# Kernel tuning notes

Measured on AMD Instinct MI355X. Metric: run time of the kernel, lower is better.

Reference implementation:

```python
import jax, jax.numpy as jnp
from jax import lax
import numpy as np

D_MODEL = 1024; N_HEADS = 16; D_K = 64; D_FF = 4096
D_STATE = 16; D_CONV = 4; D_INNER = 2048; EPS = 1e-5
BATCH = 2; SEQ = 2048


def _ln(x, g, b):
    m = x.mean(-1, keepdims=True)
    v = ((x - m) ** 2).mean(-1, keepdims=True)
    return (x - m) * lax.rsqrt(v + EPS) * g + b


def setup_inputs() -> dict:
    key = jax.random.key(0)
    ks = jax.random.split(key, 12)
    rn = lambda k, sh, s=0.02: jax.random.normal(k, sh, jnp.float32) * s
    return {
        'x': jax.random.normal(ks[0], (BATCH, SEQ, D_MODEL), jnp.float32),
        'ln1_g': jnp.ones(D_MODEL), 'ln1_b': jnp.zeros(D_MODEL),
        'Wq': rn(ks[1], (D_MODEL, D_MODEL)), 'bq': jnp.zeros(D_MODEL),
        'Wk': rn(ks[2], (D_MODEL, D_MODEL)), 'bk': jnp.zeros(D_MODEL),
        'Wv': rn(ks[3], (D_MODEL, D_MODEL)), 'bv': jnp.zeros(D_MODEL),
        'Wo': rn(ks[4], (D_MODEL, D_MODEL)), 'bo': jnp.zeros(D_MODEL),
        'ln2_g': jnp.ones(D_MODEL), 'ln2_b': jnp.zeros(D_MODEL),
        'in_w': rn(ks[5], (D_MODEL, 2 * D_INNER)), 'in_b': jnp.zeros(2 * D_INNER),
        'conv_w': rn(ks[6], (D_INNER, 1, D_CONV), 0.2), 'conv_b': jnp.zeros(D_INNER),
        'xp_w': rn(ks[7], (D_INNER, 2 * D_STATE)), 'xp_b': jnp.zeros(2 * D_STATE),
        'dt': rn(ks[8], (D_INNER,), 0.1), 'A': rn(ks[9], (D_STATE, D_STATE), 0.1),
        'Dp': jnp.ones(D_INNER),
        'out_w': rn(ks[10], (D_INNER, D_MODEL)), 'out_b': jnp.zeros(D_MODEL),
        'ln3_g': jnp.ones(D_MODEL), 'ln3_b': jnp.zeros(D_MODEL),
        'fc1_w': rn(ks[11], (D_MODEL, D_FF)), 'fc1_b': jnp.zeros(D_FF),
        'fc2_w': rn(jax.random.fold_in(key, 99), (D_FF, D_MODEL)), 'fc2_b': jnp.zeros(D_MODEL),
    }


def reference(x, ln1_g, ln1_b, Wq, bq, Wk, bk, Wv, bv, Wo, bo, ln2_g, ln2_b,
              in_w, in_b, conv_w, conv_b, xp_w, xp_b, dt, A, Dp, out_w, out_b,
              ln3_g, ln3_b, fc1_w, fc1_b, fc2_w, fc2_b):
    Bsz, S, _ = x.shape
    # --- attention (block sliding-window mask == full causal mask) ---
    h = _ln(x, ln1_g, ln1_b)
    q = (h @ Wq + bq).reshape(Bsz, S, N_HEADS, D_K).transpose(0, 2, 1, 3)
    k = (h @ Wk + bk).reshape(Bsz, S, N_HEADS, D_K).transpose(0, 2, 1, 3)
    v = (h @ Wv + bv).reshape(Bsz, S, N_HEADS, D_K).transpose(0, 2, 1, 3)
    scores = jnp.einsum('bhqd,bhkd->bhqk', q, k) / float(D_K ** 0.5)
    causal = jnp.tril(jnp.ones((S, S), bool))
    scores = jnp.where(causal, scores, -jnp.inf)
    probs = jax.nn.softmax(scores, axis=-1)
    attn = jnp.einsum('bhqk,bhkd->bhqd', probs, v).transpose(0, 2, 1, 3).reshape(Bsz, S, D_MODEL)
    x = x + attn @ Wo + bo
    # --- Mamba-style layer ---
    h = _ln(x, ln2_g, ln2_b)
    xr = h @ in_w + in_b                      # (B,S,2*Di)
    xm, res = xr[..., :D_INNER], xr[..., D_INNER:]
    # causal depthwise conv: torch Conv1d(pad=d_conv-1)[..., :S] == left-pad conv
    xc = lax.conv_general_dilated(xm.transpose(0, 2, 1), conv_w, (1,), [(D_CONV - 1, 0)],
                                  dimension_numbers=('NCH', 'OIH', 'NCH'),
                                  feature_group_count=D_INNER)
    xm = jax.nn.silu((xc + conv_b[None, :, None]).transpose(0, 2, 1))
    xdbl = xm @ xp_w + xp_b                   # (B,S,2*d_state)
    Bm, Cm = xdbl[..., :D_STATE], xdbl[..., D_STATE:]
    # dt = exp(param)[:d_state], indexed by i % d_state per step (as in source)
    dts = jnp.exp(dt)[:D_STATE][jnp.arange(S) % D_STATE]  # (S,)
    # NOTE: the source scan never uses u = x[:,i,:] (and hence D); hs depends
    # only on dt, A, B, C — replicated faithfully here.

    def step(hst, inp):
        d_t, b_t, c_t = inp
        A_t = jnp.exp(d_t * A)                # (d_state,d_state)
        hst = jnp.tanh(hst @ A_t.T) + b_t * hst + c_t
        return hst, hst

    h0 = jnp.zeros((Bsz, D_STATE), x.dtype)
    _, hs = lax.scan(step, h0, (dts, Bm.transpose(1, 0, 2), Cm.transpose(1, 0, 2)))
    hs = hs.transpose(1, 0, 2)                # (B,S,d_state)
    y = jnp.repeat(hs, D_INNER // D_STATE, axis=-1) + res
    x = x + y @ out_w + out_b
    # --- FFN (tanh-approx GELU) ---
    h = _ln(x, ln3_g, ln3_b)
    x = x + jax.nn.gelu(h @ fc1_w + fc1_b, approximate=True) @ fc2_w + fc2_b
    return x
```

## Files before the change

kernel.cpp:

```cpp
#include <hip/hip_runtime.h>
#include <hip/hip_bf16.h>


#define SEQ     2048
#define BATCH   2
#define MROWS   4096
#define DMODEL  1024
#define DINNER  2048
#define DFF     4096
#define QKVLD   3072

typedef __attribute__((ext_vector_type(8))) short bf16x8;
typedef __attribute__((ext_vector_type(4))) float f32x4;

__device__ __forceinline__ unsigned short f2b(float x){
    __hip_bfloat16 h = __float2bfloat16(x);
    return *reinterpret_cast<unsigned short*>(&h);
}
__device__ __forceinline__ float b2f(unsigned short u){
    __hip_bfloat16 h;
    *reinterpret_cast<unsigned short*>(&h) = u;
    return __bfloat162float(h);
}
__device__ __forceinline__ float b2f_lo(unsigned u){
    return __builtin_bit_cast(float, u << 16);
}
__device__ __forceinline__ float b2f_hi(unsigned u){
    return __builtin_bit_cast(float, u & 0xFFFF0000u);
}
__device__ __forceinline__ float gelu_f(float v){
    float u = 0.7978845608f*(v + 0.044715f*v*v*v);
    float e = __expf(2.f*u);
    float th = 1.f - 2.f*__builtin_amdgcn_rcpf(e + 1.f);
    return 0.5f*v*(1.f + th);
}
__device__ __forceinline__ void gload16(const unsigned short* g, unsigned short* l){
    __builtin_amdgcn_global_load_lds(
        (const __attribute__((address_space(1))) void*)g,
        (__attribute__((address_space(3))) void*)l, 16, 0, 0);
}
__device__ __forceinline__ void gload16f(const float* g, float* l){
    __builtin_amdgcn_global_load_lds(
        (const __attribute__((address_space(1))) void*)g,
        (__attribute__((address_space(3))) void*)l, 16, 0, 0);
}
template<int CTRL>
__device__ __forceinline__ float dppf(float x){
    int r = __builtin_amdgcn_mov_dpp(__builtin_bit_cast(int, x), CTRL, 0xf, 0xf, false);
    return __builtin_bit_cast(float, r);
}
template<int CTRL>
__device__ __forceinline__ int dppi(int x){
    return __builtin_amdgcn_mov_dpp(x, CTRL, 0xf, 0xf, false);
}

__global__ __launch_bounds__(256) void transpose_cast(
    const float* __restrict__ W, unsigned short* __restrict__ Wt, int K, int N)
{
    __shared__ float t[64*65];
    int n0 = blockIdx.x*64, k0 = blockIdx.y*64;
    int c = threadIdx.x & 63, r0 = threadIdx.x >> 6;
    #pragma unroll
    for (int rr = 0; rr < 64; rr += 4)
        t[(rr+r0)*65 + c] = W[(size_t)(k0+rr+r0)*N + n0 + c];
    __syncthreads();
    #pragma unroll
    for (int rr = 0; rr < 64; rr += 4)
        Wt[(size_t)(n0+rr+r0)*K + k0 + c] = f2b(t[c*65 + rr + r0]);
}

__global__ __launch_bounds__(256) void concat_bias(
    const float* __restrict__ b0, const float* __restrict__ b1,
    const float* __restrict__ b2, float* __restrict__ o)
{
    int t = blockIdx.x*256 + threadIdx.x;
    float v = (t < 1024) ? b0[t] : (t < 2048 ? b1[t-1024] : b2[t-2048]);
    o[t] = v;
}

__global__ __launch_bounds__(256) void layernorm_bf16(
    const float* __restrict__ x, const float* __restrict__ g,
    const float* __restrict__ b, unsigned short* __restrict__ out)
{
    int row = blockIdx.x;
    const float4* xr = (const float4*)(x + (size_t)row*DMODEL);
    int tid = threadIdx.x;
    float4 xv = xr[tid];
    float s  = xv.x + xv.y + xv.z + xv.w;
    float ss = xv.x*xv.x + xv.y*xv.y + xv.z*xv.z + xv.w*xv.w;
    #pragma unroll
    for (int d = 32; d > 0; d >>= 1){ s += __shfl_xor(s,d); ss += __shfl_xor(ss,d); }
    __shared__ float sm[8];
    int wv = tid>>6, ln = tid&63;
    if (ln == 0){ sm[wv] = s; sm[4+wv] = ss; }
    __syncthreads();
    s  = sm[0]+sm[1]+sm[2]+sm[3];
    ss = sm[4]+sm[5]+sm[6]+sm[7];
    float mean = s*(1.f/DMODEL);
    float var  = ss*(1.f/DMODEL) - mean*mean;
    float rstd = rsqrtf(var + 1e-5f);
    float4 gv = ((const float4*)g)[tid];
    float4 bv = ((const float4*)b)[tid];
    ushort4 o;
    o.x = f2b((xv.x-mean)*rstd*gv.x + bv.x);
    o.y = f2b((xv.y-mean)*rstd*gv.y + bv.y);
    o.z = f2b((xv.z-mean)*rstd*gv.z + bv.z);
    o.w = f2b((xv.w-mean)*rstd*gv.w + bv.w);
    ((ushort4*)(out + (size_t)row*DMODEL))[tid] = o;
}

template<int BN, int OUT_BF16, int HAS_RES, int ACT>
__global__ __launch_bounds__(256,2) void gemm_bt(
    const unsigned short* __restrict__ A, const unsigned short* __restrict__ Bt,
    const float* __restrict__ bias, const float* __restrict__ res,
    void* __restrict__ outp, int Ndim, int Kdim)
{
    constexpr int NT = BN/32;
    constexpr int BROWS = BN/32;
    __shared__ unsigned short As[128*64];
    __shared__ unsigned short Bs[BN*64];
    int tid = threadIdx.x;
    int lane = tid & 63, wv = tid >> 6;
    int l15 = lane & 15, quad = lane >> 4;
    int m0 = blockIdx.y*128, n0 = blockIdx.x*BN;
    int mo = (wv>>1)*64, no = (wv&1)*(BN/2);
    int rsub = (lane >> 3);
    int cc8  = (lane & 7)*8;
    f32x4 zz = {0.f,0.f,0.f,0.f};
    f32x4 acc[4][NT];
    #pragma unroll
    for (int i=0;i<4;++i)
      #pragma unroll
      for (int j=0;j<NT;++j) acc[i][j] = zz;

    for (int k0 = 0; k0 < Kdim; k0 += 64){
        const unsigned short* Ab = A  + (size_t)(m0 + wv*32 + rsub)*Kdim + k0 + cc8;
        const unsigned short* Bb = Bt + (size_t)(n0 + wv*(BN/4) + rsub)*Kdim + k0 + cc8;
        #pragma unroll
        for (int i=0;i<4;++i)
            gload16(Ab + (size_t)(i*8)*Kdim, &As[(wv*32 + i*8)*64]);
        #pragma unroll
        for (int i=0;i<BROWS;++i)
            gload16(Bb + (size_t)(i*8)*Kdim, &Bs[(wv*(BN/4) + i*8)*64]);
        __syncthreads();
        #pragma unroll
        for (int kc=0;kc<2;++kc){
            bf16x8 af[4], bfr[NT];
            #pragma unroll
            for (int t=0;t<4;++t)
                af[t]  = *(const bf16x8*)(&As[(mo + t*16 + l15)*64 + kc*32 + quad*8]);
            #pragma unroll
            for (int t=0;t<NT;++t)
                bfr[t] = *(const bf16x8*)(&Bs[(no + t*16 + l15)*64 + kc*32 + quad*8]);
            #pragma unroll
            for (int mt=0;mt<4;++mt)
              #pragma unroll
              for (int nt=0;nt<NT;++nt)
                acc[mt][nt] = __builtin_amdgcn_mfma_f32_16x16x32_bf16(af[mt], bfr[nt], acc[mt][nt], 0,0,0);
        }
        __syncthreads();
    }
    #pragma unroll
    for (int mt=0;mt<4;++mt){
      #pragma unroll
      for (int nt=0;nt<NT;++nt){
        int gn = n0 + no + nt*16 + l15;
        float bval = bias[gn];
        #pragma unroll
        for (int r=0;r<4;++r){
            int gm = m0 + mo + mt*16 + quad*4 + r;
            size_t off = (size_t)gm*Ndim + gn;
            float v = acc[mt][nt][r] + bval;
            if constexpr (HAS_RES) v += res[off];
            if constexpr (ACT == 1) v = gelu_f(v);
            if constexpr (OUT_BF16) ((unsigned short*)outp)[off] = f2b(v);
            else                    ((float*)outp)[off] = v;
        }
      }
    }
}

__global__ __launch_bounds__(256,2) void attn_flash(
    const unsigned short* __restrict__ qkv, unsigned short* __restrict__ attn)
{
    __shared__ unsigned short Qs[64*72];
    __shared__ unsigned short Ks[64*72];
    __shared__ unsigned short Vt[64*72];
    __shared__ unsigned short Ps[64*72];
    int bh = blockIdx.y;
    int qt = (int)gridDim.x - 1 - (int)blockIdx.x;
    int q0 = qt*64;
    int tid = threadIdx.x, wv = tid>>6, lane = tid&63;
    int l15 = lane&15, quad = lane>>4;
    const size_t basei = (size_t)(bh>>4)*SEQ*QKVLD + (size_t)(bh&15)*64;
    const unsigned short* q = qkv + basei;
    const unsigned short* k = qkv + basei + DMODEL;
    const unsigned short* v = qkv + basei + 2*DMODEL;
    const size_t baseo = (size_t)(bh>>4)*SEQ*DMODEL + (size_t)(bh&15)*64;

    #pragma unroll
    for (int i=0;i<2;++i){
        int cch = tid + i*256; int r = cch>>3, cc = cch&7;
        *(uint4*)(&Qs[r*72 + cc*8]) = *(const uint4*)(q + (size_t)(q0+r)*QKVLD + cc*8);
    }
    __syncthreads();
    bf16x8 aq0 = *(const bf16x8*)(&Qs[(wv*16 + l15)*72 + quad*8]);
    bf16x8 aq1 = *(const bf16x8*)(&Qs[(wv*16 + l15)*72 + 32 + quad*8]);

    float m_i[4], l_i[4];
    f32x4 zz = {0.f,0.f,0.f,0.f};
    f32x4 o[4];
    #pragma unroll
    for (int r=0;r<4;++r){ m_i[r] = -__builtin_inff(); l_i[r] = 0.f; }
    #pragma unroll
    for (int d=0;d<4;++d) o[d] = zz;

    for (int kt = 0; kt <= qt; ++kt){
        int t0 = kt*64;
        #pragma unroll
        for (int i=0;i<2;++i){
            int cch = tid + i*256; int r = cch>>3, cc = cch&7;
            *(uint4*)(&Ks[r*72 + cc*8]) = *(const uint4*)(k + (size_t)(t0+r)*QKVLD + cc*8);
            uint4 vv = *(const uint4*)(v + (size_t)(t0+r)*QKVLD + cc*8);
            const unsigned short* pv = (const unsigned short*)&vv;
            #pragma unroll
            for (int j=0;j<8;++j) Vt[(cc*8+j)*72 + r] = pv[j];
        }
        __syncthreads();

        f32x4 sc[4];
        #pragma unroll
        for (int st=0;st<4;++st){
            bf16x8 b0 = *(const bf16x8*)(&Ks[(st*16+l15)*72 + quad*8]);
            bf16x8 b1 = *(const bf16x8*)(&Ks[(st*16+l15)*72 + 32 + quad*8]);
            sc[st] = __builtin_amdgcn_mfma_f32_16x16x32_bf16(aq0, b0, zz, 0,0,0);
            sc[st] = __builtin_amdgcn_mfma_f32_16x16x32_bf16(aq1, b1, sc[st], 0,0,0);
        }
        bool diag = (kt == qt);
        float sval[4][4];
        float mrow[4];
        #pragma unroll
        for (int r=0;r<4;++r) mrow[r] = -__builtin_inff();
        #pragma unroll
        for (int st=0;st<4;++st)
          #pragma unroll
          for (int r=0;r<4;++r){
            float svv = sc[st][r]*0.125f;
            if (diag && (st*16 + l15 > wv*16 + quad*4 + r)) svv = -__builtin_inff();
            sval[st][r] = svv;
            mrow[r] = fmaxf(mrow[r], svv);
          }
        #pragma unroll
        for (int d=1; d<16; d<<=1)
          #pragma unroll
          for (int r=0;r<4;++r) mrow[r] = fmaxf(mrow[r], __shfl_xor(mrow[r], d));
        float alpha[4], rsum[4];
        #pragma unroll
        for (int r=0;r<4;++r){
            float mn = fmaxf(m_i[r], mrow[r]);
            alpha[r] = __expf(m_i[r] - mn);
            m_i[r] = mn;
        }
        #pragma unroll
        for (int st=0;st<4;++st)
          #pragma unroll
          for (int r=0;r<4;++r) sval[st][r] = __expf(sval[st][r] - m_i[r]);
        #pragma unroll
        for (int r=0;r<4;++r) rsum[r] = sval[0][r]+sval[1][r]+sval[2][r]+sval[3][r];
        #pragma unroll
        for (int d=1; d<16; d<<=1)
          #pragma unroll
          for (int r=0;r<4;++r) rsum[r] += __shfl_xor(rsum[r], d);
        #pragma unroll
        for (int r=0;r<4;++r) l_i[r] = l_i[r]*alpha[r] + rsum[r];
        #pragma unroll
        for (int st=0;st<4;++st)
          #pragma unroll
          for (int r=0;r<4;++r)
            Ps[(wv*16 + quad*4 + r)*72 + st*16 + l15] = f2b(sval[st][r]);
        #pragma unroll
        for (int d=0;d<4;++d)
          #pragma unroll
          for (int r=0;r<4;++r) o[d][r] = o[d][r]*alpha[r];
        __syncthreads();
        bf16x8 ap0 = *(const bf16x8*)(&Ps[(wv*16 + l15)*72 + quad*8]);
        bf16x8 ap1 = *(const bf16x8*)(&Ps[(wv*16 + l15)*72 + 32 + quad*8]);
        #pragma unroll
        for (int dtile=0;dtile<4;++dtile){
            bf16x8 b0 = *(const bf16x8*)(&Vt[(dtile*16+l15)*72 + quad*8]);
            bf16x8 b1 = *(const bf16x8*)(&Vt[(dtile*16+l15)*72 + 32 + quad*8]);
            o[dtile] = __builtin_amdgcn_mfma_f32_16x16x32_bf16(ap0, b0, o[dtile], 0,0,0);
            o[dtile] = __builtin_amdgcn_mfma_f32_16x16x32_bf16(ap1, b1, o[dtile], 0,0,0);
        }
        __syncthreads();
    }
    #pragma unroll
    for (int r=0;r<4;++r){
        float inv = 1.f/l_i[r];
        int gm = q0 + wv*16 + quad*4 + r;
        #pragma unroll
        for (int dtile=0;dtile<4;++dtile)
            attn[baseo + (size_t)gm*DMODEL + dtile*16 + l15] = f2b(o[dtile][r]*inv);
    }
}

__global__ __launch_bounds__(256) void conv_silu(
    const unsigned short* __restrict__ xr, const float* __restrict__ cw,
    const float* __restrict__ cb, unsigned short* __restrict__ xm2)
{
    int idx = blockIdx.x*256 + threadIdx.x;
    int r  = idx >> 10;
    int c2 = (idx & 1023)*2;
    int s  = r & (SEQ-1);
    float4 w0 = *(const float4*)(cw + c2*4);
    float4 w1 = *(const float4*)(cw + (c2+1)*4);
    float w0a[4] = {w0.x,w0.y,w0.z,w0.w};
    float w1a[4] = {w1.x,w1.y,w1.z,w1.w};
    float a0 = cb[c2], a1 = cb[c2+1];
    const unsigned short* xrow = xr + (size_t)r*DFF + c2;
    #pragma unroll
    for (int j=0;j<4;++j){
        int sp = s - 3 + j;
        if (sp >= 0){
            int off = (j-3)*DFF;
            unsigned int u = *(const unsigned int*)(xrow + off);
            a0 += w0a[j]*b2f(u & 0xffff);
            a1 += w1a[j]*b2f(u >> 16);
        }
    }
    float s0 = a0 * __builtin_amdgcn_rcpf(1.f + __expf(-a0));
    float s1 = a1 * __builtin_amdgcn_rcpf(1.f + __expf(-a1));
    unsigned int op = (unsigned int)f2b(s0) | ((unsigned int)f2b(s1) << 16);
    *(unsigned int*)(xm2 + (size_t)r*DINNER + c2) = op;
}

__global__ __launch_bounds__(256) void xp_gemm(
    const unsigned short* __restrict__ xm2, const float* __restrict__ w,
    const float* __restrict__ bias, float* __restrict__ xdbl)
{
    int tid = threadIdx.x;
    int lr = tid >> 5, n = tid & 31;
    int row = blockIdx.x*8 + lr;
    const unsigned short* ar = xm2 + (size_t)row*DINNER;
    float acc = bias[n];
    #pragma unroll 4
    for (int k2 = 0; k2 < DINNER; k2 += 2){
        unsigned int u = *(const unsigned int*)(ar + k2);
        acc += b2f(u & 0xffff)*w[k2*32 + n] + b2f(u >> 16)*w[(k2+1)*32 + n];
    }
    int nc = (n < 16) ? 2*n : 2*(n-16)+1;
    xdbl[(size_t)row*32 + nc] = acc;
}

__device__ __forceinline__ float scan_step_pk(float h, const unsigned (&Wp)[8],
                                              float bv, float cv)
{
    float r1  = dppf<0x121>(h);
    float r2  = dppf<0x122>(h);
    float r3  = dppf<0x123>(h);
    float r4  = dppf<0x124>(h);
    float r5  = dppf<0x125>(h);
    float r6  = dppf<0x126>(h);
    float r7  = dppf<0x127>(h);
    float r8  = dppf<0x128>(h);
    float r9  = dppf<0x129>(h);
    float r10 = dppf<0x12a>(h);
    float r11 = dppf<0x12b>(h);
    float r12 = dppf<0x12c>(h);
    float r13 = dppf<0x12d>(h);
    float r14 = dppf<0x12e>(h);
    float r15 = dppf<0x12f>(h);
    float a0 = b2f_lo(Wp[0])*h;
    a0 = fmaf(b2f_hi(Wp[0]), r1, a0);
    a0 = fmaf(b2f_lo(Wp[1]), r2, a0);
    a0 = fmaf(b2f_hi(Wp[1]), r3, a0);
    float a1 = b2f_lo(Wp[2])*r4;
    a1 = fmaf(b2f_hi(Wp[2]), r5, a1);
    a1 = fmaf(b2f_lo(Wp[3]), r6, a1);
    a1 = fmaf(b2f_hi(Wp[3]), r7, a1);
    float a2 = b2f_lo(Wp[4])*r8;
    a2 = fmaf(b2f_hi(Wp[4]), r9, a2);
    a2 = fmaf(b2f_lo(Wp[5]), r10, a2);
    a2 = fmaf(b2f_hi(Wp[5]), r11, a2);
    float a3 = b2f_lo(Wp[6])*r12;
    a3 = fmaf(b2f_hi(Wp[6]), r13, a3);
    a3 = fmaf(b2f_lo(Wp[7]), r14, a3);
    a3 = fmaf(b2f_hi(Wp[7]), r15, a3);
    float x = (a0+a1)+(a2+a3);
    float e2 = __expf(x);
    float th = 1.f - 2.f*__builtin_amdgcn_rcpf(e2 + 1.f);
    return th + fmaf(bv, h, cv);
}

__global__ __launch_bounds__(128,1) void scan_k(
    const float* __restrict__ xdbl, const float* __restrict__ dt,
    const float* __restrict__ A, float* __restrict__ hsT)
{
    __shared__ float bc[2][2][64*32];
    int tid = threadIdx.x;
    int wv = tid >> 6, lane = tid & 63;
    int i = lane & 15;
    int b = wv;

    int c[16];
    c[0]  = i;
    c[1]  = dppi<0x121>(i);
    c[2]  = dppi<0x122>(i);
    c[3]  = dppi<0x123>(i);
    c[4]  = dppi<0x124>(i);
    c[5]  = dppi<0x125>(i);
    c[6]  = dppi<0x126>(i);
    c[7]  = dppi<0x127>(i);
    c[8]  = dppi<0x128>(i);
    c[9]  = dppi<0x129>(i);
    c[10] = dppi<0x12a>(i);
    c[11] = dppi<0x12b>(i);
    c[12] = dppi<0x12c>(i);
    c[13] = dppi<0x12d>(i);
    c[14] = dppi<0x12e>(i);
    c[15] = dppi<0x12f>(i);

    unsigned Wpk[16][8];
    #pragma unroll
    for (int p=0;p<16;++p){
        float dtp = __expf(dt[p]);
        #pragma unroll
        for (int jj=0;jj<8;++jj){
            float w0 = 2.f*__expf(dtp * A[i*16 + c[2*jj]]);
            float w1 = 2.f*__expf(dtp * A[i*16 + c[2*jj+1]]);
            Wpk[p][jj] = (unsigned)f2b(w0) | ((unsigned)f2b(w1) << 16);
        }
    }

    {
        const float* src = xdbl + (size_t)(b*SEQ)*32 + lane*4;
        #pragma unroll
        for (int k=0;k<8;++k)
            gload16f(src + k*256, &bc[wv][0][k*256]);
    }
    __builtin_amdgcn_s_waitcnt(0x0F70);

    float hn = 0.f;
    float h0s=0.f, h1s=0.f, h2s=0.f;
    for (int chunk = 0; chunk < 32; ++chunk){
        if (chunk < 31){
            const float* nsrc = xdbl + (size_t)(b*SEQ + (chunk+1)*64)*32 + lane*4;
            float* nb = &bc[wv][(chunk+1)&1][0];
            #pragma unroll
            for (int k=0;k<8;++k)
                gload16f(nsrc + k*256, nb + k*256);
        }
        const float* cur = &bc[wv][chunk&1][0];
        float* hp = hsT + (size_t)(b*16 + i)*SEQ + chunk*64;
        float2 bc0 = *(const float2*)(cur + 2*i);
        float2 bc1 = *(const float2*)(cur + 32 + 2*i);
        #pragma unroll
        for (int st=0; st<64; ++st){
            float bv = bc0.x, cv = bc0.y;
            bc0 = bc1;
            if (st < 62)
                bc1 = *(const float2*)(cur + (st+2)*32 + 2*i);
            hn = scan_step_pk(hn, Wpk[st & 15], bv, cv);
            if ((st&3)==0)      h0s = hn;
            else if ((st&3)==1) h1s = hn;
            else if ((st&3)==2) h2s = hn;
            else if (lane < 16){
                float4 o4 = {h0s, h1s, h2s, hn};
                *(float4*)(hp + (st-3)) = o4;
            }
        }
        __builtin_amdgcn_s_waitcnt(0x0F70);
    }
}

__global__ __launch_bounds__(256) void y_assemble(
    const float* __restrict__ hsT, const unsigned short* __restrict__ xr,
    unsigned short* __restrict__ y)
{
    int idx = blockIdx.x*256 + threadIdx.x;
    int r = idx >> 10;
    int c2 = (idx & 1023)*2;
    int bb = r >> 11, s = r & (SEQ-1);
    unsigned int u = *(const unsigned int*)(xr + (size_t)r*DFF + DINNER + c2);
    float h0 = hsT[(size_t)(bb*16 + (c2 >> 7))*SEQ + s];
    float y0 = h0 + b2f(u & 0xffff);
    float y1 = h0 + b2f(u >> 16);
    *(unsigned int*)(y + (size_t)r*DINNER + c2) =
        (unsigned int)f2b(y0) | ((unsigned int)f2b(y1) << 16);
}

extern "C" void kernel_launch(void* const* d_in, const int* in_sizes, int n_in,
                              void* d_out, int out_size, void* d_ws, size_t ws_size,
                              hipStream_t stream)
{
    (void)in_sizes; (void)n_in; (void)out_size; (void)ws_size;
    const float* x     = (const float*)d_in[0];
    const float* ln1_g = (const float*)d_in[1];
    const float* ln1_b = (const float*)d_in[2];
    const float* Wq    = (const float*)d_in[3];
    const float* bq    = (const float*)d_in[4];
    const float* Wk    = (const float*)d_in[5];
    const float* bk    = (const float*)d_in[6];
    const float* Wv    = (const float*)d_in[7];
    const float* bv    = (const float*)d_in[8];
    const float* Wo    = (const float*)d_in[9];
    const float* bo    = (const float*)d_in[10];
    const float* ln2_g = (const float*)d_in[11];
    const float* ln2_b = (const float*)d_in[12];
    const float* in_w  = (const float*)d_in[13];
    const float* in_b  = (const float*)d_in[14];
    const float* conv_w= (const float*)d_in[15];
    const float* conv_b= (const float*)d_in[16];
    const float* xp_w  = (const float*)d_in[17];
    const float* xp_b  = (const float*)d_in[18];
    const float* dt    = (const float*)d_in[19];
    const float* A     = (const float*)d_in[20];
    const float* out_w = (const float*)d_in[22];
    const float* out_b = (const float*)d_in[23];
    const float* ln3_g = (const float*)d_in[24];
    const float* ln3_b = (const float*)d_in[25];
    const float* fc1_w = (const float*)d_in[26];
    const float* fc1_b = (const float*)d_in[27];
    const float* fc2_w = (const float*)d_in[28];
    const float* fc2_b = (const float*)d_in[29];

    char* ws = (char*)d_ws;
    const size_t MB = 1ull << 20;
    unsigned short* qkvT = (unsigned short*)(ws + 0*MB);
    unsigned short* WoT  = (unsigned short*)(ws + 6*MB);
    unsigned short* inT  = (unsigned short*)(ws + 8*MB);
    unsigned short* outT = (unsigned short*)(ws + 16*MB);
    unsigned short* f1T  = (unsigned short*)(ws + 20*MB);
    unsigned short* f2T  = (unsigned short*)(ws + 28*MB);
    unsigned short* hbf  = (unsigned short*)(ws + 36*MB);
    float*          x2   = (float*)(ws + 44*MB);
    float*          x3   = (float*)(ws + 60*MB);
    unsigned short* qkv  = (unsigned short*)(ws + 76*MB);
    unsigned short* attnb= (unsigned short*)(ws + 100*MB);
    unsigned short* xr   = (unsigned short*)(ws + 76*MB);
    unsigned short* ffn  = (unsigned short*)(ws + 76*MB);
    unsigned short* xm2  = (unsigned short*)(ws + 108*MB);
    unsigned short* yb   = (unsigned short*)(ws + 108*MB);
    float*          xdbl = (float*)(ws + 124*MB);
    float*          hsb  = (float*)(ws + 124*MB + 512*1024);
    float*          bqkv = (float*)(ws + 125*MB);

    dim3 blk(256);
    transpose_cast<<<dim3(16,16), blk, 0, stream>>>(Wq, qkvT,              1024, 1024);
    transpose_cast<<<dim3(16,16), blk, 0, stream>>>(Wk, qkvT + 1024*1024,  1024, 1024);
    transpose_cast<<<dim3(16,16), blk, 0, stream>>>(Wv, qkvT + 2*1024*1024,1024, 1024);
    transpose_cast<<<dim3(16,16), blk, 0, stream>>>(Wo, WoT, 1024, 1024);
    transpose_cast<<<dim3(64,16), blk, 0, stream>>>(in_w, inT, 1024, 4096);
    transpose_cast<<<dim3(16,32), blk, 0, stream>>>(out_w, outT, 2048, 1024);
    transpose_cast<<<dim3(64,16), blk, 0, stream>>>(fc1_w, f1T, 1024, 4096);
    transpose_cast<<<dim3(16,64), blk, 0, stream>>>(fc2_w, f2T, 4096, 1024);
    concat_bias<<<12, blk, 0, stream>>>(bq, bk, bv, bqkv);

    layernorm_bf16<<<MROWS, blk, 0, stream>>>(x, ln1_g, ln1_b, hbf);
    gemm_bt<128,1,0,0><<<dim3(24,32), blk, 0, stream>>>(hbf, qkvT, bqkv, nullptr, qkv, QKVLD, 1024);
    attn_flash<<<dim3(32,32), blk, 0, stream>>>(qkv, attnb);
    gemm_bt<64,0,1,0><<<dim3(16,32), blk, 0, stream>>>(attnb, WoT, bo, x, x2, 1024, 1024);
    layernorm_bf16<<<MROWS, blk, 0, stream>>>(x2, ln2_g, ln2_b, hbf);
    gemm_bt<128,1,0,0><<<dim3(32,32), blk, 0, stream>>>(hbf, inT, in_b, nullptr, xr, 4096, 1024);
    conv_silu<<<16384, blk, 0, stream>>>(xr, conv_w, conv_b, xm2);
    xp_gemm<<<512, blk, 0, stream>>>(xm2, xp_w, xp_b, xdbl);
    scan_k<<<1, dim3(128), 0, stream>>>(xdbl, dt, A, hsb);
    y_assemble<<<16384, blk, 0, stream>>>(hsb, xr, yb);
    gemm_bt<64,0,1,0><<<dim3(16,32), blk, 0, stream>>>(yb, outT, out_b, x2, x3, 1024, 2048);
    layernorm_bf16<<<MROWS, blk, 0, stream>>>(x3, ln3_g, ln3_b, hbf);
    gemm_bt<128,1,0,1><<<dim3(32,32), blk, 0, stream>>>(hbf, f1T, fc1_b, nullptr, ffn, 4096, 1024);
    gemm_bt<64,0,1,0><<<dim3(16,32), blk, 0, stream>>>(ffn, f2T, fc2_b, x3, (float*)d_out, 1024, 4096);
}
```

Baseline: 997.1 us.

## Use packed fp16 dot2 and DPP pairs in serial scan step, register-prefetch inputs

Rewrites the per-step recurrence of the sequential scan to pack the state into fp16 pairs. It shuffles them with 7 DPP moves instead of 15 and accumulates with v_dot2 instructions. The weights are pre-scaled so that exp2 can replace exp, and the tanh is folded into one rcp plus one fma. The LDS double-buffer for B/C is replaced by direct global loads into register banks that are prefetched 16 steps ahead. The aim is to shorten the latency-bound critical path of the serial scan, at the cost of fp16 rounding of the state and weights.

```diff
diff --git a/kernel.cpp b/kernel.cpp
--- a/kernel.cpp
+++ b/kernel.cpp
@@ -12,6 +12,7 @@
 
 typedef __attribute__((ext_vector_type(8))) short bf16x8;
 typedef __attribute__((ext_vector_type(4))) float f32x4;
+typedef __attribute__((ext_vector_type(2))) __fp16 f16x2;
 
 __device__ __forceinline__ unsigned short f2b(float x){
     __hip_bfloat16 h = __float2bfloat16(x);
@@ -21,12 +22,6 @@
     __hip_bfloat16 h;
     *reinterpret_cast<unsigned short*>(&h) = u;
     return __bfloat162float(h);
-}
-__device__ __forceinline__ float b2f_lo(unsigned u){
-    return __builtin_bit_cast(float, u << 16);
-}
-__device__ __forceinline__ float b2f_hi(unsigned u){
-    return __builtin_bit_cast(float, u & 0xFFFF0000u);
 }
 __device__ __forceinline__ float gelu_f(float v){
     float u = 0.7978845608f*(v + 0.044715f*v*v*v);
@@ -39,11 +34,6 @@
         (const __attribute__((address_space(1))) void*)g,
         (__attribute__((address_space(3))) void*)l, 16, 0, 0);
 }
-__device__ __forceinline__ void gload16f(const float* g, float* l){
-    __builtin_amdgcn_global_load_lds(
-        (const __attribute__((address_space(1))) void*)g,
-        (__attribute__((address_space(3))) void*)l, 16, 0, 0);
-}
 template<int CTRL>
 __device__ __forceinline__ float dppf(float x){
     int r = __builtin_amdgcn_mov_dpp(__builtin_bit_cast(int, x), CTRL, 0xf, 0xf, false);
@@ -52,6 +42,27 @@
 template<int CTRL>
 __device__ __forceinline__ int dppi(int x){
     return __builtin_amdgcn_mov_dpp(x, CTRL, 0xf, 0xf, false);
+}
+template<int CTRL>
+__device__ __forceinline__ f16x2 dpp_h2(f16x2 x){
+    int r = __builtin_amdgcn_mov_dpp(__builtin_bit_cast(int, x), CTRL, 0xf, 0xf, false);
+    return __builtin_bit_cast(f16x2, r);
+}
+
+#if __has_builtin(__builtin_amdgcn_exp2f)
+#define W_SCALE 2.8853900817779268f
+__device__ __forceinline__ float exp_2s(float x){ return __builtin_amdgcn_exp2f(x); }
+#else
+#define W_SCALE 2.0f
+__device__ __forceinline__ float exp_2s(float x){ return __expf(x); }
+#endif
+
+__device__ __forceinline__ float hdot2(f16x2 a, f16x2 b, float c){
+#if __has_builtin(__builtin_amdgcn_fdot2)
+    return __builtin_amdgcn_fdot2(a, b, c, false);
+#else
+    return c + (float)a[0]*(float)b[0] + (float)a[1]*(float)b[1];
+#endif
 }
 
 __global__ __launch_bounds__(256) void transpose_cast(
@@ -352,124 +363,99 @@
     xdbl[(size_t)row*32 + nc] = acc;
 }
 
-__device__ __forceinline__ float scan_step_pk(float h, const unsigned (&Wp)[8],
-                                              float bv, float cv)
-{
-    float r1  = dppf<0x121>(h);
-    float r2  = dppf<0x122>(h);
-    float r3  = dppf<0x123>(h);
-    float r4  = dppf<0x124>(h);
-    float r5  = dppf<0x125>(h);
-    float r6  = dppf<0x126>(h);
-    float r7  = dppf<0x127>(h);
-    float r8  = dppf<0x128>(h);
-    float r9  = dppf<0x129>(h);
-    float r10 = dppf<0x12a>(h);
-    float r11 = dppf<0x12b>(h);
-    float r12 = dppf<0x12c>(h);
-    float r13 = dppf<0x12d>(h);
-    float r14 = dppf<0x12e>(h);
-    float r15 = dppf<0x12f>(h);
-    float a0 = b2f_lo(Wp[0])*h;
-    a0 = fmaf(b2f_hi(Wp[0]), r1, a0);
-    a0 = fmaf(b2f_lo(Wp[1]), r2, a0);
-    a0 = fmaf(b2f_hi(Wp[1]), r3, a0);
-    float a1 = b2f_lo(Wp[2])*r4;
-    a1 = fmaf(b2f_hi(Wp[2]), r5, a1);
-    a1 = fmaf(b2f_lo(Wp[3]), r6, a1);
-    a1 = fmaf(b2f_hi(Wp[3]), r7, a1);
-    float a2 = b2f_lo(Wp[4])*r8;
-    a2 = fmaf(b2f_hi(Wp[4]), r9, a2);
-    a2 = fmaf(b2f_lo(Wp[5]), r10, a2);
-    a2 = fmaf(b2f_hi(Wp[5]), r11, a2);
-    float a3 = b2f_lo(Wp[6])*r12;
-    a3 = fmaf(b2f_hi(Wp[6]), r13, a3);
-    a3 = fmaf(b2f_lo(Wp[7]), r14, a3);
-    a3 = fmaf(b2f_hi(Wp[7]), r15, a3);
-    float x = (a0+a1)+(a2+a3);
-    float e2 = __expf(x);
-    float th = 1.f - 2.f*__builtin_amdgcn_rcpf(e2 + 1.f);
-    return th + fmaf(bv, h, cv);
+__device__ __forceinline__ float scan_step_dot(float h, const f16x2 (&Wp)[8],
+                                               float bv, float cv)
+{
+    float rr = dppf<0x121>(h);
+    f16x2 p0 = __builtin_amdgcn_cvt_pkrtz(h, rr);
+    f16x2 p1 = dpp_h2<0x122>(p0);
+    f16x2 p2 = dpp_h2<0x124>(p0);
+    f16x2 p3 = dpp_h2<0x126>(p0);
+    f16x2 p4 = dpp_h2<0x128>(p0);
+    f16x2 p5 = dpp_h2<0x12a>(p0);
+    f16x2 p6 = dpp_h2<0x12c>(p0);
+    f16x2 p7 = dpp_h2<0x12e>(p0);
+    float a0 = hdot2(Wp[0], p0, 0.f);
+    a0 = hdot2(Wp[1], p1, a0);
+    a0 = hdot2(Wp[2], p2, a0);
+    a0 = hdot2(Wp[3], p3, a0);
+    float a1 = hdot2(Wp[4], p4, 0.f);
+    a1 = hdot2(Wp[5], p5, a1);
+    a1 = hdot2(Wp[6], p6, a1);
+    a1 = hdot2(Wp[7], p7, a1);
+    float u  = fmaf(bv, h, cv + 1.f);
+    float e2 = exp_2s(a0 + a1);
+    float r  = __builtin_amdgcn_rcpf(e2 + 1.f);
+    return fmaf(-2.f, r, u);
+}
+
+__device__ __forceinline__ void load_bank(float2 (&bk)[16], const float* src){
+    #pragma unroll
+    for (int j=0;j<16;++j) bk[j] = *(const float2*)(src + (size_t)j*32);
+}
+
+__device__ __forceinline__ void compute16(const float2 (&bk)[16],
+                                          const f16x2 (&Wf)[16][8],
+                                          float& hn, float* hp, int lane)
+{
+    float h0s=0.f, h1s=0.f, h2s=0.f;
+    #pragma unroll
+    for (int j=0;j<16;++j){
+        hn = scan_step_dot(hn, Wf[j], bk[j].x, bk[j].y);
+        if ((j&3)==0)      h0s = hn;
+        else if ((j&3)==1) h1s = hn;
+        else if ((j&3)==2) h2s = hn;
+        else if (lane < 16){
+            float4 o4 = {h0s, h1s, h2s, hn};
+            *(float4*)(hp + j - 3) = o4;
+        }
+    }
 }
 
 __global__ __launch_bounds__(128,1) void scan_k(
     const float* __restrict__ xdbl, const float* __restrict__ dt,
     const float* __restrict__ A, float* __restrict__ hsT)
 {
-    __shared__ float bc[2][2][64*32];
     int tid = threadIdx.x;
-    int wv = tid >> 6, lane = tid & 63;
+    int lane = tid & 63;
+    int b = tid >> 6;
     int i = lane & 15;
-    int b = wv;
-
-    int c[16];
-    c[0]  = i;
-    c[1]  = dppi<0x121>(i);
-    c[2]  = dppi<0x122>(i);
-    c[3]  = dppi<0x123>(i);
-    c[4]  = dppi<0x124>(i);
-    c[5]  = dppi<0x125>(i);
-    c[6]  = dppi<0x126>(i);
-    c[7]  = dppi<0x127>(i);
-    c[8]  = dppi<0x128>(i);
-    c[9]  = dppi<0x129>(i);
-    c[10] = dppi<0x12a>(i);
-    c[11] = dppi<0x12b>(i);
-    c[12] = dppi<0x12c>(i);
-    c[13] = dppi<0x12d>(i);
-    c[14] = dppi<0x12e>(i);
-    c[15] = dppi<0x12f>(i);
-
-    unsigned Wpk[16][8];
+
+    int c1 = dppi<0x121>(i);
+    int sj[8], tj[8];
+    sj[0] = i;               tj[0] = c1;
+    sj[1] = dppi<0x122>(i);  tj[1] = dppi<0x122>(c1);
+    sj[2] = dppi<0x124>(i);  tj[2] = dppi<0x124>(c1);
+    sj[3] = dppi<0x126>(i);  tj[3] = dppi<0x126>(c1);
+    sj[4] = dppi<0x128>(i);  tj[4] = dppi<0x128>(c1);
+    sj[5] = dppi<0x12a>(i);  tj[5] = dppi<0x12a>(c1);
+    sj[6] = dppi<0x12c>(i);  tj[6] = dppi<0x12c>(c1);
+    sj[7] = dppi<0x12e>(i);  tj[7] = dppi<0x12e>(c1);
+
+    f16x2 Wf[16][8];
     #pragma unroll
     for (int p=0;p<16;++p){
         float dtp = __expf(dt[p]);
         #pragma unroll
         for (int jj=0;jj<8;++jj){
-            float w0 = 2.f*__expf(dtp * A[i*16 + c[2*jj]]);
-            float w1 = 2.f*__expf(dtp * A[i*16 + c[2*jj+1]]);
-            Wpk[p][jj] = (unsigned)f2b(w0) | ((unsigned)f2b(w1) << 16);
-        }
-    }
-
-    {
-        const float* src = xdbl + (size_t)(b*SEQ)*32 + lane*4;
-        #pragma unroll
-        for (int k=0;k<8;++k)
-            gload16f(src + k*256, &bc[wv][0][k*256]);
-    }
-    __builtin_amdgcn_s_waitcnt(0x0F70);
-
+            float w0 = W_SCALE*__expf(dtp * A[i*16 + sj[jj]]);
+            float w1 = W_SCALE*__expf(dtp * A[i*16 + tj[jj]]);
+            Wf[p][jj] = __builtin_amdgcn_cvt_pkrtz(w0, w1);
+        }
+    }
+
+    const float* src = xdbl + (size_t)(b*SEQ)*32 + 2*i;
+    float* hp = hsT + (size_t)(b*16 + i)*SEQ;
+    float2 bA[16], bB[16];
+    load_bank(bA, src);
     float hn = 0.f;
-    float h0s=0.f, h1s=0.f, h2s=0.f;
-    for (int chunk = 0; chunk < 32; ++chunk){
-        if (chunk < 31){
-            const float* nsrc = xdbl + (size_t)(b*SEQ + (chunk+1)*64)*32 + lane*4;
-            float* nb = &bc[wv][(chunk+1)&1][0];
-            #pragma unroll
-            for (int k=0;k<8;++k)
-                gload16f(nsrc + k*256, nb + k*256);
-        }
-        const float* cur = &bc[wv][chunk&1][0];
-        float* hp = hsT + (size_t)(b*16 + i)*SEQ + chunk*64;
-        float2 bc0 = *(const float2*)(cur + 2*i);
-        float2 bc1 = *(const float2*)(cur + 32 + 2*i);
-        #pragma unroll
-        for (int st=0; st<64; ++st){
-            float bv = bc0.x, cv = bc0.y;
-            bc0 = bc1;
-            if (st < 62)
-                bc1 = *(const float2*)(cur + (st+2)*32 + 2*i);
-            hn = scan_step_pk(hn, Wpk[st & 15], bv, cv);
-            if ((st&3)==0)      h0s = hn;
-            else if ((st&3)==1) h1s = hn;
-            else if ((st&3)==2) h2s = hn;
-            else if (lane < 16){
-                float4 o4 = {h0s, h1s, h2s, hn};
-                *(float4*)(hp + (st-3)) = o4;
-            }
-        }
-        __builtin_amdgcn_s_waitcnt(0x0F70);
+    for (int bp = 0; bp < 64; ++bp){
+        int t0 = bp*32;
+        load_bank(bB, src + (size_t)(t0+16)*32);
+        compute16(bA, Wf, hn, hp + t0, lane);
+        int t2 = (bp < 63) ? (t0 + 32) : 0;
+        load_bank(bA, src + (size_t)t2*32);
+        compute16(bB, Wf, hn, hp + t0 + 16, lane);
     }
 }
 
```

Result: faster. 930.3 us (-6.7%).
